# Performance work log

Measured on AMD Instinct MI355X. Metric: run time of the kernel, lower is better.

## Reference

```python
import jax, jax.numpy as jnp
import numpy as np

B, S, D, H, HD, FF, L, NF, NC, DH = 262144, 6, 16, 4, 4, 64, 10, 6, 139, 32
EPS = 1e-5

def _ln(x, w, b):
    m = x.mean(-1, keepdims=True)
    v = ((x - m) ** 2).mean(-1, keepdims=True)
    return (x - m) / jnp.sqrt(v + EPS) * w + b

def setup_inputs() -> dict:
    key = jax.random.key(0)
    ks = iter(jax.random.split(key, 64))
    def rn(shape, s=0.1):
        return jax.random.normal(next(ks), shape, jnp.float32) * s
    inp = {
        'feature_ids': jax.random.randint(next(ks), (B, S), 0, NF, jnp.int32),
        'feature_values': jax.random.normal(next(ks), (B, S, 1), jnp.float32),
        'mask': jnp.ones((B, S), bool),
        'type_embed': rn((NF, D), 1.0),
        'value_w': rn((D, 1)), 'value_b': rn((D,)),
        'pos_enc': rn((NF, D), 1.0),
        'qkv_w': rn((2, 3 * D, D)), 'qkv_b': rn((2, 3 * D)),
        'out_w': rn((2, D, D)), 'out_b': rn((2, D)),
        'ln1_w': jnp.ones((2, D)), 'ln1_b': jnp.zeros((2, D)),
        'ffn_w1': rn((2, FF, D)), 'ffn_b1': rn((2, FF)),
        'ffn_w2': rn((2, D, FF)), 'ffn_b2': rn((2, D)),
        'ln2_w': jnp.ones((2, D)), 'ln2_b': jnp.zeros((2, D)),
        'pool_w': rn((D, D)), 'pool_b': rn((D,)),
        'mu_w': rn((L, D)), 'mu_b': rn((L,)),
        'lv_w': rn((L, D)), 'lv_b': rn((L,)),
        'dec_w1': rn((NF, DH, L)), 'dec_b1': rn((NF, DH)),
        'dec_w2': rn((NF, 1, DH)), 'dec_b2': rn((NF, 1)),
        'cls_w1': rn((32, L)), 'cls_b1': rn((32,)),
        'cls_w2': rn((NC, 32)), 'cls_b2': rn((NC,)),
    }
    return inp

def _forward(feature_ids, feature_values, mask, type_embed, value_w, value_b, pos_enc,
             qkv_w, qkv_b, out_w, out_b, ln1_w, ln1_b, ffn_w1, ffn_b1, ffn_w2, ffn_b2,
             ln2_w, ln2_b, pool_w, pool_b, mu_w, mu_b, lv_w, lv_b,
             dec_w1, dec_b1, dec_w2, dec_b2, cls_w1, cls_b1, cls_w2, cls_b2):
    x = type_embed[feature_ids] + feature_values @ value_w.T + value_b  # (B,S,D)
    x = x + pos_enc[None, :S]
    maskf = mask.astype(x.dtype)
    bias = jnp.where(mask, 0.0, -1e9)[:, None, None, :]  # (B,1,1,S)
    for l in range(2):
        qkv = x @ qkv_w[l].T + qkv_b[l]
        q, k, v = jnp.split(qkv, 3, axis=-1)
        q = q.reshape(B, S, H, HD).transpose(0, 2, 1, 3)
        k = k.reshape(B, S, H, HD).transpose(0, 2, 1, 3)
        v = v.reshape(B, S, H, HD).transpose(0, 2, 1, 3)
        sc = jnp.einsum('bhqd,bhkd->bhqk', q, k) / jnp.sqrt(jnp.float32(HD))
        a = jax.nn.softmax(sc + bias, axis=-1)
        o = jnp.einsum('bhqk,bhkd->bhqd', a, v).transpose(0, 2, 1, 3).reshape(B, S, D)
        x = _ln(x + (o @ out_w[l].T + out_b[l]), ln1_w[l], ln1_b[l])
        f = jax.nn.relu(x @ ffn_w1[l].T + ffn_b1[l]) @ ffn_w2[l].T + ffn_b2[l]
        x = _ln(x + f, ln2_w[l], ln2_b[l])
    pooled = (x * maskf[..., None]).sum(1) / maskf.sum(1, keepdims=True)
    pooled = jax.nn.relu(pooled @ pool_w.T + pool_b)
    mu = pooled @ mu_w.T + mu_b
    logvar = pooled @ lv_w.T + lv_b
    eps = jax.random.normal(jax.random.key(42), mu.shape, mu.dtype)
    z = mu + eps * jnp.exp(0.5 * logvar)
    # run all 6 tiny decoders densely, then gather per feature_id (same math as per-token dispatch)
    h = jax.nn.relu(jnp.einsum('ehl,bl->beh', dec_w1, z) + dec_b1)      # (B,6,DH)
    allo = jnp.einsum('eoh,beh->beo', dec_w2, h)[..., 0] + dec_b2[:, 0]  # (B,6)
    recons = jnp.take_along_axis(allo, feature_ids, axis=1)[..., None]   # (B,S,1)
    logits = jax.nn.relu(z @ cls_w1.T + cls_b1) @ cls_w2.T + cls_b2
    return recons, mu, logvar, logits

def reference(feature_ids, feature_values, mask, type_embed, value_w, value_b, pos_enc,
              qkv_w, qkv_b, out_w, out_b, ln1_w, ln1_b, ffn_w1, ffn_b1, ffn_w2, ffn_b2,
              ln2_w, ln2_b, pool_w, pool_b, mu_w, mu_b, lv_w, lv_b,
              dec_w1, dec_b1, dec_w2, dec_b2, cls_w1, cls_b1, cls_w2, cls_b2):
    return _forward(feature_ids, feature_values, mask, type_embed, value_w, value_b, pos_enc,
                    qkv_w, qkv_b, out_w, out_b, ln1_w, ln1_b, ffn_w1, ffn_b1, ffn_w2, ffn_b2,
                    ln2_w, ln2_b, pool_w, pool_b, mu_w, mu_b, lv_w, lv_b,
                    dec_w1, dec_b1, dec_w2, dec_b2, cls_w1, cls_b1, cls_w2, cls_b2)
```

## Files before the change

kernel.cpp:

```cpp
#include <hip/hip_runtime.h>

#define DEVINL __device__ __forceinline__

constexpr int B  = 262144;
constexpr int S  = 6;
constexpr int NC = 139;

typedef _Float16 h2v __attribute__((ext_vector_type(2)));

constexpr int OUTB  = 0;
constexpr int LN1W  = 32;
constexpr int LN1B  = 64;
constexpr int LN2W  = 96;
constexpr int LN2B  = 128;
constexpr int QKVB  = 160;
constexpr int FF1B  = 256;
constexpr int FF2B  = 384;
constexpr int POOLB = 416;
constexpr int MUB   = 432;
constexpr int LVB   = 444;
constexpr int CL1B  = 456;
constexpr int CL2B  = 488;
constexpr int DEC1B = 628;
constexpr int DEC2W = 820;
constexpr int DEC2B = 1012;
constexpr int VALW  = 1020;
constexpr int VALB  = 1036;
constexpr int HQKV  = 1052;
constexpr int HOUT  = 1820;
constexpr int HFF1  = 2076;
constexpr int HFF2  = 3100;
constexpr int HPOOL = 4124;
constexpr int HMUW  = 4252;
constexpr int HLVW  = 4332;
constexpr int HCL1  = 4412;
constexpr int HCL2  = 4668;
constexpr int HDEC1 = 6892;
constexpr int WS_FLOATS = 8428;

#define LD4(off) (*reinterpret_cast<const float4*>(&smem[(off)]))
#define LD2(off) (*reinterpret_cast<const float2*>(&smem[(off)]))
#define BCH(f)   __builtin_bit_cast(h2v, (f))
#define BCF(h)   __builtin_bit_cast(float, (h))
#define FDOT2(a, b, c) __builtin_amdgcn_fdot2((a), (b), (c), false)

DEVINL h2v mkh2(float a, float b) { h2v r; r.x = (_Float16)a; r.y = (_Float16)b; return r; }
DEVINL h2v pkrtz(float a, float b) {
  return __builtin_bit_cast(h2v, __builtin_amdgcn_cvt_pkrtz(a, b));
}

#define DOTH_3(xh, bas, acc) do {                                    \
  const float4 wa_ = LD4(bas);                                       \
  const float4 wb_ = LD4((bas) + 4);                                 \
  const h2v w0_ = BCH(wa_.x), w1_ = BCH(wa_.y), w2_ = BCH(wa_.z), w3_ = BCH(wa_.w); \
  const h2v w4_ = BCH(wb_.x), w5_ = BCH(wb_.y), w6_ = BCH(wb_.z), w7_ = BCH(wb_.w); \
  _Pragma("unroll")                                                  \
  for (int r_ = 0; r_ < 3; ++r_) {                                   \
    acc[r_] = FDOT2(xh[r_][0], w0_, acc[r_]);                        \
    acc[r_] = FDOT2(xh[r_][1], w1_, acc[r_]);                        \
    acc[r_] = FDOT2(xh[r_][2], w2_, acc[r_]);                        \
    acc[r_] = FDOT2(xh[r_][3], w3_, acc[r_]);                        \
    acc[r_] = FDOT2(xh[r_][4], w4_, acc[r_]);                        \
    acc[r_] = FDOT2(xh[r_][5], w5_, acc[r_]);                        \
    acc[r_] = FDOT2(xh[r_][6], w6_, acc[r_]);                        \
    acc[r_] = FDOT2(xh[r_][7], w7_, acc[r_]);                        \
  }                                                                  \
} while (0)

#define DOT8H(vh, bas, acc) do {                                     \
  const float4 wa_ = LD4(bas);                                       \
  const float4 wb_ = LD4((bas) + 4);                                 \
  acc = FDOT2(vh[0], BCH(wa_.x), acc);                               \
  acc = FDOT2(vh[1], BCH(wa_.y), acc);                               \
  acc = FDOT2(vh[2], BCH(wa_.z), acc);                               \
  acc = FDOT2(vh[3], BCH(wa_.w), acc);                               \
  acc = FDOT2(vh[4], BCH(wb_.x), acc);                               \
  acc = FDOT2(vh[5], BCH(wb_.y), acc);                               \
  acc = FDOT2(vh[6], BCH(wb_.z), acc);                               \
  acc = FDOT2(vh[7], BCH(wb_.w), acc);                               \
} while (0)

DEVINL float dppswap(float v) {
  return __int_as_float(__builtin_amdgcn_mov_dpp(__float_as_int(v), 0xB1, 0xF, 0xF, true));
}

DEVINL float jax_normal_part(unsigned i) {
  const unsigned k1 = 42u;
  const unsigned k2 = 0x1BD11BDAu ^ 42u;
  unsigned x0 = 0u;
  unsigned x1 = i + k1;
#define TFR(r) { x0 += x1; x1 = (x1 << (r)) | (x1 >> (32 - (r))); x1 ^= x0; }
  TFR(13) TFR(15) TFR(26) TFR(6)
  x0 += k1; x1 += k2 + 1u;
  TFR(17) TFR(29) TFR(16) TFR(24)
  x0 += k2; x1 += 0u + 2u;
  TFR(13) TFR(15) TFR(26) TFR(6)
  x0 += 0u; x1 += k1 + 3u;
  TFR(17) TFR(29) TFR(16) TFR(24)
  x0 += k1; x1 += k2 + 4u;
  TFR(13) TFR(15) TFR(26) TFR(6)
  x0 += k2; x1 += 0u + 5u;
#undef TFR
  unsigned bits = x0 ^ x1;
  unsigned fb = (bits >> 9) | 0x3f800000u;
  float f = __uint_as_float(fb) - 1.0f;
  const float lo = -0.99999994f;
  float u = fmaxf(lo, fmaf(f, 2.0f, lo));
  float w = -log1pf(-u * u);
  float p;
  if (w < 5.0f) {
    w -= 2.5f;
    p =  2.81022636e-08f;
    p = fmaf(p, w,  3.43273939e-07f);
    p = fmaf(p, w, -3.5233877e-06f);
    p = fmaf(p, w, -4.39150654e-06f);
    p = fmaf(p, w,  0.00021858087f);
    p = fmaf(p, w, -0.00125372503f);
    p = fmaf(p, w, -0.00417768164f);
    p = fmaf(p, w,  0.246640727f);
    p = fmaf(p, w,  1.50140941f);
  } else {
    w = sqrtf(w) - 3.0f;
    p = -0.000200214257f;
    p = fmaf(p, w,  0.000100950558f);
    p = fmaf(p, w,  0.00134934322f);
    p = fmaf(p, w, -0.00367342844f);
    p = fmaf(p, w,  0.00573950773f);
    p = fmaf(p, w, -0.0076224613f);
    p = fmaf(p, w,  0.00943887047f);
    p = fmaf(p, w,  1.00167406f);
    p = fmaf(p, w,  2.83297682f);
  }
  return 1.41421356237f * (p * u);
}

__global__ __launch_bounds__(256, 2) void vae_fwd(
    const int*   __restrict__ feature_ids,
    const float* __restrict__ feature_values,
    const float* __restrict__ type_embed,
    const float* __restrict__ value_w,
    const float* __restrict__ value_b,
    const float* __restrict__ pos_enc,
    const float* __restrict__ qkv_w,
    const float* __restrict__ qkv_b,
    const float* __restrict__ out_w,
    const float* __restrict__ out_b,
    const float* __restrict__ ln1_w, const float* __restrict__ ln1_b,
    const float* __restrict__ ffn_w1,
    const float* __restrict__ ffn_b1,
    const float* __restrict__ ffn_w2,
    const float* __restrict__ ffn_b2,
    const float* __restrict__ ln2_w, const float* __restrict__ ln2_b,
    const float* __restrict__ pool_w,
    const float* __restrict__ pool_b,
    const float* __restrict__ mu_w, const float* __restrict__ mu_b,
    const float* __restrict__ lv_w, const float* __restrict__ lv_b,
    const float* __restrict__ dec_w1,
    const float* __restrict__ dec_b1,
    const float* __restrict__ dec_w2,
    const float* __restrict__ dec_b2,
    const float* __restrict__ cls_w1,
    const float* __restrict__ cls_b1,
    const float* __restrict__ cls_w2,
    const float* __restrict__ cls_b2,
    float*       __restrict__ out)
{
  __shared__ __align__(16) float smem[WS_FLOATS];

  {
    const int t = threadIdx.x;
#define CP(dst, src, n) for (int i_ = t; i_ < (n); i_ += 256) smem[(dst) + i_] = (src)[i_]
#define CPH(dst, src, n) for (int i_ = t; i_ < (n); i_ += 256) \
    smem[(dst) + i_] = BCF(mkh2((src)[2 * i_], (src)[2 * i_ + 1]))
    CP(OUTB, out_b, 32);
    CP(LN1W, ln1_w, 32);  CP(LN1B, ln1_b, 32);
    CP(LN2W, ln2_w, 32);  CP(LN2B, ln2_b, 32);
    CP(QKVB, qkv_b, 96);
    CP(FF1B, ffn_b1, 128); CP(FF2B, ffn_b2, 32);
    CP(POOLB, pool_b, 16);
    CP(MUB, mu_b, 10);    CP(LVB, lv_b, 10);
    CP(CL1B, cls_b1, 32); CP(CL2B, cls_b2, 139);
    CP(DEC1B, dec_b1, 192); CP(DEC2W, dec_w2, 192); CP(DEC2B, dec_b2, 6);
    CP(VALW, value_w, 16); CP(VALB, value_b, 16);
    CPH(HQKV, qkv_w, 768);
    CPH(HOUT, out_w, 256);
    CPH(HFF1, ffn_w1, 1024);
    CPH(HFF2, ffn_w2, 1024);
    CPH(HPOOL, pool_w, 128);
    CPH(HMUW, mu_w, 80);
    CPH(HLVW, lv_w, 80);
    CPH(HCL2, cls_w2, 2224);
    for (int idx = t; idx < 256; idx += 256) {
      int row = idx >> 3, k = idx & 7;
      float a = (k < 5) ? cls_w1[row * 10 + 2 * k] : 0.f;
      float b = (k < 5) ? cls_w1[row * 10 + 2 * k + 1] : 0.f;
      smem[HCL1 + idx] = BCF(mkh2(a, b));
    }
    for (int idx = t; idx < 1536; idx += 256) {
      int row = idx >> 3, k = idx & 7;
      float a = (k < 5) ? dec_w1[row * 10 + 2 * k] : 0.f;
      float b = (k < 5) ? dec_w1[row * 10 + 2 * k + 1] : 0.f;
      smem[HDEC1 + idx] = BCF(mkh2(a, b));
    }
#undef CP
#undef CPH
  }
  __syncthreads();

  const int tid  = blockIdx.x * 256 + threadIdx.x;
  const int elem = tid >> 1;
  const int sub  = tid & 1;
  const bool his = (sub != 0);

  float x[3][16];
  int   fid[3];
#pragma unroll
  for (int i = 0; i < 3; ++i) {
    const int r = sub * 3 + i;
    fid[i] = feature_ids[elem * S + r];
    const float fv = feature_values[elem * S + r];
    const float* te = type_embed + fid[i] * 16;
    const float* pe = pos_enc + r * 16;
#pragma unroll
    for (int d = 0; d < 16; ++d)
      x[i][d] = te[d] + fv * smem[VALW + d] + smem[VALB + d] + pe[d];
  }

#pragma unroll 1
  for (int l = 0; l < 2; ++l) {
    const int WqH = HQKV + l * 384;
    const int bqO = QKVB + l * 48;
    const int WoH = HOUT + l * 128;
    const int w1H = HFF1 + l * 512;
    const int b1O = FF1B + l * 64;
    const int w2H = HFF2 + l * 512;
    const int b2O = FF2B + l * 16;

    h2v xh[3][8];
#pragma unroll
    for (int r = 0; r < 3; ++r)
#pragma unroll
      for (int k = 0; k < 8; ++k) xh[r][k] = pkrtz(x[r][2 * k], x[r][2 * k + 1]);

    float y[3][16];
#pragma unroll
    for (int r = 0; r < 3; ++r)
#pragma unroll
      for (int j = 0; j < 16; ++j) y[r][j] = x[r][j] + smem[OUTB + l * 16 + j];

#pragma unroll 1
    for (int h = 0; h < 4; ++h) {
      float qq[4][3], kk[4][3];
#pragma unroll
      for (int e = 0; e < 4; ++e) {
        float bq0 = smem[bqO + h * 4 + e];
        float bk0 = smem[bqO + 16 + h * 4 + e];
        float aq[3] = {bq0, bq0, bq0};
        float ak[3] = {bk0, bk0, bk0};
        DOTH_3(xh, WqH + (h * 4 + e) * 8, aq);
        DOTH_3(xh, WqH + (16 + h * 4 + e) * 8, ak);
#pragma unroll
        for (int r = 0; r < 3; ++r) { qq[e][r] = aq[r] * 0.5f; kk[e][r] = ak[r]; }
      }

      h2v qp[3][2], kpo[3][2], kpp[3][2];
#pragma unroll
      for (int r = 0; r < 3; ++r) {
        qp[r][0] = pkrtz(qq[0][r], qq[1][r]);
        qp[r][1] = pkrtz(qq[2][r], qq[3][r]);
      }
#pragma unroll
      for (int i = 0; i < 3; ++i) {
        kpo[i][0] = pkrtz(kk[0][i], kk[1][i]);
        kpo[i][1] = pkrtz(kk[2][i], kk[3][i]);
        kpp[i][0] = BCH(dppswap(BCF(kpo[i][0])));
        kpp[i][1] = BCH(dppswap(BCF(kpo[i][1])));
      }

      float scO[3][3], scP[3][3];
#pragma unroll
      for (int r = 0; r < 3; ++r)
#pragma unroll
        for (int i = 0; i < 3; ++i) {
          scO[r][i] = FDOT2(qp[r][1], kpo[i][1], FDOT2(qp[r][0], kpo[i][0], 0.f));
          scP[r][i] = FDOT2(qp[r][1], kpp[i][1], FDOT2(qp[r][0], kpp[i][0], 0.f));
        }

#pragma unroll
      for (int r = 0; r < 3; ++r) {
        float mx = scO[r][0];
#pragma unroll
        for (int i = 1; i < 3; ++i) mx = fmaxf(mx, scO[r][i]);
#pragma unroll
        for (int i = 0; i < 3; ++i) mx = fmaxf(mx, scP[r][i]);
        float den = 0.f;
#pragma unroll
        for (int i = 0; i < 3; ++i) { scO[r][i] = __expf(scO[r][i] - mx); den += scO[r][i]; }
#pragma unroll
        for (int i = 0; i < 3; ++i) { scP[r][i] = __expf(scP[r][i] - mx); den += scP[r][i]; }
        const float inv = 1.0f / den;
#pragma unroll
        for (int i = 0; i < 3; ++i) { scO[r][i] *= inv; scP[r][i] *= inv; }
      }

      float vv[4][3];
#pragma unroll
      for (int e = 0; e < 4; ++e) {
        float bv0 = smem[bqO + 32 + h * 4 + e];
        float av[3] = {bv0, bv0, bv0};
        DOTH_3(xh, WqH + (32 + h * 4 + e) * 8, av);
#pragma unroll
        for (int r = 0; r < 3; ++r) vv[e][r] = av[r];
      }

      h2v vp0[4], vp1[4], vp2[4];
#pragma unroll
      for (int e = 0; e < 4; ++e) {
        const float q0 = dppswap(vv[e][0]);
        const float q1 = dppswap(vv[e][1]);
        const float q2 = dppswap(vv[e][2]);
        vp0[e] = pkrtz(vv[e][0], vv[e][1]);
        vp1[e] = pkrtz(vv[e][2], q0);
        vp2[e] = pkrtz(q1, q2);
      }
      h2v sp0[3], sp1[3], sp2[3];
#pragma unroll
      for (int r = 0; r < 3; ++r) {
        sp0[r] = pkrtz(scO[r][0], scO[r][1]);
        sp1[r] = pkrtz(scO[r][2], scP[r][0]);
        sp2[r] = pkrtz(scP[r][1], scP[r][2]);
      }
      float oh[3][4];
#pragma unroll
      for (int r = 0; r < 3; ++r)
#pragma unroll
        for (int e = 0; e < 4; ++e)
          oh[r][e] = FDOT2(sp2[r], vp2[e], FDOT2(sp1[r], vp1[e], FDOT2(sp0[r], vp0[e], 0.f)));

      h2v ohp[3][2];
#pragma unroll
      for (int r = 0; r < 3; ++r) {
        ohp[r][0] = pkrtz(oh[r][0], oh[r][1]);
        ohp[r][1] = pkrtz(oh[r][2], oh[r][3]);
      }
      const int wbase = WoH + h * 2;
#pragma unroll
      for (int j = 0; j < 16; ++j) {
        const float2 w = LD2(wbase + j * 8);
        const h2v w0 = BCH(w.x), w1 = BCH(w.y);
#pragma unroll
        for (int r = 0; r < 3; ++r)
          y[r][j] = FDOT2(ohp[r][1], w1, FDOT2(ohp[r][0], w0, y[r][j]));
      }
    }

#pragma unroll
    for (int r = 0; r < 3; ++r) {
      float m = 0.f;
#pragma unroll
      for (int d = 0; d < 16; ++d) m += y[r][d];
      m *= 0.0625f;
      float var = 0.f;
#pragma unroll
      for (int d = 0; d < 16; ++d) { float dd = y[r][d] - m; var = fmaf(dd, dd, var); }
      var *= 0.0625f;
      float rr = 1.0f / sqrtf(var + 1e-5f);
#pragma unroll
      for (int d = 0; d < 16; ++d)
        y[r][d] = (y[r][d] - m) * rr * smem[LN1W + l * 16 + d] + smem[LN1B + l * 16 + d];
    }

    h2v yh[3][8];
#pragma unroll
    for (int r = 0; r < 3; ++r)
#pragma unroll
      for (int k = 0; k < 8; ++k) yh[r][k] = pkrtz(y[r][2 * k], y[r][2 * k + 1]);

    float t2[3][16];
#pragma unroll
    for (int r = 0; r < 3; ++r)
#pragma unroll
      for (int j = 0; j < 16; ++j) t2[r][j] = y[r][j] + smem[b2O + j];

#pragma unroll 1
    for (int fo = 0; fo < 4; ++fo) {
      h2v hch[3][8];
#pragma unroll
      for (int m2 = 0; m2 < 8; ++m2) {
        float b0 = smem[b1O + fo * 16 + 2 * m2];
        float b1v = smem[b1O + fo * 16 + 2 * m2 + 1];
        float a0[3] = {b0, b0, b0};
        float a1[3] = {b1v, b1v, b1v};
        DOTH_3(yh, w1H + (fo * 16 + 2 * m2) * 8, a0);
        DOTH_3(yh, w1H + (fo * 16 + 2 * m2 + 1) * 8, a1);
#pragma unroll
        for (int r = 0; r < 3; ++r)
          hch[r][m2] = pkrtz(fmaxf(a0[r], 0.f), fmaxf(a1[r], 0.f));
      }
#pragma unroll
      for (int j = 0; j < 16; ++j) {
        const int bas = w2H + j * 32 + fo * 8;
        float a[3] = {t2[0][j], t2[1][j], t2[2][j]};
        DOTH_3(hch, bas, a);
        t2[0][j] = a[0]; t2[1][j] = a[1]; t2[2][j] = a[2];
      }
    }
#pragma unroll
    for (int r = 0; r < 3; ++r) {
      float m = 0.f;
#pragma unroll
      for (int d = 0; d < 16; ++d) m += t2[r][d];
      m *= 0.0625f;
      float var = 0.f;
#pragma unroll
      for (int d = 0; d < 16; ++d) { float dd = t2[r][d] - m; var = fmaf(dd, dd, var); }
      var *= 0.0625f;
      float rr = 1.0f / sqrtf(var + 1e-5f);
#pragma unroll
      for (int d = 0; d < 16; ++d)
        x[r][d] = (t2[r][d] - m) * rr * smem[LN2W + l * 16 + d] + smem[LN2B + l * 16 + d];
    }
  }

  float pooled[16];
#pragma unroll
  for (int d = 0; d < 16; ++d) {
    float v = x[0][d] + x[1][d] + x[2][d];
    v += dppswap(v);
    pooled[d] = v * (1.0f / 6.0f);
  }
  h2v ph[8];
#pragma unroll
  for (int k = 0; k < 8; ++k) ph[k] = pkrtz(pooled[2 * k], pooled[2 * k + 1]);

  float pp[16];
#pragma unroll
  for (int jj = 0; jj < 8; ++jj) {
    const int j = sub * 8 + jj;
    float a = smem[POOLB + j];
    DOT8H(ph, HPOOL + j * 8, a);
    a = fmaxf(a, 0.f);
    const float o = dppswap(a);
    pp[jj]     = his ? o : a;
    pp[8 + jj] = his ? a : o;
  }
  h2v pph[8];
#pragma unroll
  for (int k = 0; k < 8; ++k) pph[k] = pkrtz(pp[2 * k], pp[2 * k + 1]);

  float* muo = out + (size_t)B * 6;
  float* lvo = out + (size_t)B * 16;
  float z5[5];
#pragma unroll
  for (int jj = 0; jj < 5; ++jj) {
    const int j = sub * 5 + jj;
    float mu = smem[MUB + j], lv = smem[LVB + j];
    DOT8H(pph, HMUW + j * 8, mu);
    DOT8H(pph, HLVW + j * 8, lv);
    const float eps = jax_normal_part((unsigned)elem * 10u + (unsigned)j);
    z5[jj] = fmaf(eps, __expf(0.5f * lv), mu);
    muo[(size_t)elem * 10 + j] = mu;
    lvo[(size_t)elem * 10 + j] = lv;
  }

  float z[10];
#pragma unroll
  for (int jj = 0; jj < 5; ++jj) {
    const float o = dppswap(z5[jj]);
    z[jj]     = his ? o : z5[jj];
    z[5 + jj] = his ? z5[jj] : o;
  }
  h2v zh8[8];
#pragma unroll
  for (int k = 0; k < 5; ++k) zh8[k] = pkrtz(z[2 * k], z[2 * k + 1]);
  zh8[5] = pkrtz(0.f, 0.f); zh8[6] = zh8[5]; zh8[7] = zh8[5];

  float h2[32];
#pragma unroll
  for (int ii = 0; ii < 16; ++ii) {
    const int i = sub * 16 + ii;
    float a = smem[CL1B + i];
    DOT8H(zh8, HCL1 + i * 8, a);
    a = fmaxf(a, 0.f);
    const float o = dppswap(a);
    h2[ii]      = his ? o : a;
    h2[16 + ii] = his ? a : o;
  }
  h2v hh[16];
#pragma unroll
  for (int k = 0; k < 16; ++k) hh[k] = pkrtz(h2[2 * k], h2[2 * k + 1]);

  float* lgo = out + (size_t)B * 26;
#pragma unroll 2
  for (int cc = 0; cc < 70; ++cc) {
    const int c = cc * 2 + sub;
    if (c < NC) {
      const int bas = HCL2 + c * 16;
      float a = smem[CL2B + c];
#pragma unroll
      for (int q4 = 0; q4 < 4; ++q4) {
        const float4 w = LD4(bas + q4 * 4);
        a = FDOT2(hh[q4 * 4 + 0], BCH(w.x), a);
        a = FDOT2(hh[q4 * 4 + 1], BCH(w.y), a);
        a = FDOT2(hh[q4 * 4 + 2], BCH(w.z), a);
        a = FDOT2(hh[q4 * 4 + 3], BCH(w.w), a);
      }
      lgo[(size_t)elem * 139 + c] = a;
    }
  }

  float accd[3];
#pragma unroll
  for (int i = 0; i < 3; ++i) {
    const int e = sub * 3 + i;
    float acc = smem[DEC2B + e];
#pragma unroll 2
    for (int dd = 0; dd < 32; ++dd) {
      float a = smem[DEC1B + e * 32 + dd];
      DOT8H(zh8, HDEC1 + (e * 32 + dd) * 8, a);
      acc = fmaf(fmaxf(a, 0.f), smem[DEC2W + e * 32 + dd], acc);
    }
    accd[i] = acc;
  }
  float alo[3], ahi[3];
#pragma unroll
  for (int i = 0; i < 3; ++i) {
    const float o = dppswap(accd[i]);
    alo[i] = his ? o : accd[i];
    ahi[i] = his ? accd[i] : o;
  }
#pragma unroll
  for (int i = 0; i < 3; ++i) {
    const int f = fid[i];
    float v = alo[0];
    v = (f == 1) ? alo[1] : v;
    v = (f == 2) ? alo[2] : v;
    v = (f == 3) ? ahi[0] : v;
    v = (f == 4) ? ahi[1] : v;
    v = (f == 5) ? ahi[2] : v;
    out[(size_t)elem * 6 + sub * 3 + i] = v;
  }
}

extern "C" void kernel_launch(void* const* d_in, const int* in_sizes, int n_in,
                              void* d_out, int out_size, void* d_ws, size_t ws_size,
                              hipStream_t stream) {
  (void)in_sizes; (void)n_in; (void)d_ws; (void)ws_size; (void)out_size;
  const int*   feature_ids    = (const int*)  d_in[0];
  const float* feature_values = (const float*)d_in[1];
  const float* type_embed = (const float*)d_in[3];
  const float* value_w    = (const float*)d_in[4];
  const float* value_b    = (const float*)d_in[5];
  const float* pos_enc    = (const float*)d_in[6];
  const float* qkv_w      = (const float*)d_in[7];
  const float* qkv_b      = (const float*)d_in[8];
  const float* out_w      = (const float*)d_in[9];
  const float* out_b      = (const float*)d_in[10];
  const float* ln1_w      = (const float*)d_in[11];
  const float* ln1_b      = (const float*)d_in[12];
  const float* ffn_w1     = (const float*)d_in[13];
  const float* ffn_b1     = (const float*)d_in[14];
  const float* ffn_w2     = (const float*)d_in[15];
  const float* ffn_b2     = (const float*)d_in[16];
  const float* ln2_w      = (const float*)d_in[17];
  const float* ln2_b      = (const float*)d_in[18];
  const float* pool_w     = (const float*)d_in[19];
  const float* pool_b     = (const float*)d_in[20];
  const float* mu_w       = (const float*)d_in[21];
  const float* mu_b       = (const float*)d_in[22];
  const float* lv_w       = (const float*)d_in[23];
  const float* lv_b       = (const float*)d_in[24];
  const float* dec_w1     = (const float*)d_in[25];
  const float* dec_b1     = (const float*)d_in[26];
  const float* dec_w2     = (const float*)d_in[27];
  const float* dec_b2     = (const float*)d_in[28];
  const float* cls_w1     = (const float*)d_in[29];
  const float* cls_b1     = (const float*)d_in[30];
  const float* cls_w2     = (const float*)d_in[31];
  const float* cls_b2     = (const float*)d_in[32];
  float* outp = (float*)d_out;

  const int threads = 256;
  const int blocks  = (B * 2) / threads;
  vae_fwd<<<blocks, threads, 0, stream>>>(
      feature_ids, feature_values, type_embed, value_w, value_b, pos_enc,
      qkv_w, qkv_b, out_w, out_b, ln1_w, ln1_b, ffn_w1, ffn_b1, ffn_w2, ffn_b2,
      ln2_w, ln2_b, pool_w, pool_b, mu_w, mu_b, lv_w, lv_b,
      dec_w1, dec_b1, dec_w2, dec_b2, cls_w1, cls_b1, cls_w2, cls_b2, outp);
}
```

Before: 294.2 us.

## Prepack classifier and decoder fp16 weights into global workspace, read via cache

Adds a small prepack kernel that converts cls_w2 and dec_w1 to packed fp16 in the workspace buffer. The main kernel now reads these weights from global memory (L1/L2 cached) instead of staging them in LDS. This roughly halves shared memory per block, which cuts per-block staging work and may raise occupancy. The cost is that the hot classifier and decoder loops now issue global vector loads instead of LDS reads, and there is an extra kernel launch.

After: 307.0 us. 1.04x slower.

```diff
diff --git a/kernel.cpp b/kernel.cpp
--- a/kernel.cpp
+++ b/kernel.cpp
@@ -34,9 +34,11 @@
 constexpr int HMUW  = 4252;
 constexpr int HLVW  = 4332;
 constexpr int HCL1  = 4412;
-constexpr int HCL2  = 4668;
-constexpr int HDEC1 = 6892;
-constexpr int WS_FLOATS = 8428;
+constexpr int WS_FLOATS = 4668;
+
+constexpr int WSCL2  = 0;
+constexpr int WSDEC1 = 2224;
+constexpr int WS_U32 = 3760;
 
 #define LD4(off) (*reinterpret_cast<const float4*>(&smem[(off)]))
 #define LD2(off) (*reinterpret_cast<const float2*>(&smem[(off)]))
@@ -70,6 +72,19 @@
 #define DOT8H(vh, bas, acc) do {                                     \
   const float4 wa_ = LD4(bas);                                       \
   const float4 wb_ = LD4((bas) + 4);                                 \
+  acc = FDOT2(vh[0], BCH(wa_.x), acc);                               \
+  acc = FDOT2(vh[1], BCH(wa_.y), acc);                               \
+  acc = FDOT2(vh[2], BCH(wa_.z), acc);                               \
+  acc = FDOT2(vh[3], BCH(wa_.w), acc);                               \
+  acc = FDOT2(vh[4], BCH(wb_.x), acc);                               \
+  acc = FDOT2(vh[5], BCH(wb_.y), acc);                               \
+  acc = FDOT2(vh[6], BCH(wb_.z), acc);                               \
+  acc = FDOT2(vh[7], BCH(wb_.w), acc);                               \
+} while (0)
+
+#define DOT8G(vh, p, acc) do {                                       \
+  const float4 wa_ = (p)[0];                                         \
+  const float4 wb_ = (p)[1];                                         \
   acc = FDOT2(vh[0], BCH(wa_.x), acc);                               \
   acc = FDOT2(vh[1], BCH(wa_.y), acc);                               \
   acc = FDOT2(vh[2], BCH(wa_.z), acc);                               \
@@ -134,6 +149,22 @@
   return 1.41421356237f * (p * u);
 }
 
+__global__ __launch_bounds__(256) void prepack_ws(
+    const float* __restrict__ cls_w2,
+    const float* __restrict__ dec_w1,
+    unsigned*    __restrict__ ws)
+{
+  const int t = blockIdx.x * 256 + threadIdx.x;
+  for (int i = t; i < 2224; i += 2048)
+    ws[WSCL2 + i] = __builtin_bit_cast(unsigned, mkh2(cls_w2[2 * i], cls_w2[2 * i + 1]));
+  for (int i = t; i < 1536; i += 2048) {
+    int row = i >> 3, k = i & 7;
+    float a = (k < 5) ? dec_w1[row * 10 + 2 * k] : 0.f;
+    float b = (k < 5) ? dec_w1[row * 10 + 2 * k + 1] : 0.f;
+    ws[WSDEC1 + i] = __builtin_bit_cast(unsigned, mkh2(a, b));
+  }
+}
+
 __global__ __launch_bounds__(256, 2) void vae_fwd(
     const int*   __restrict__ feature_ids,
     const float* __restrict__ feature_values,
@@ -155,14 +186,13 @@
     const float* __restrict__ pool_b,
     const float* __restrict__ mu_w, const float* __restrict__ mu_b,
     const float* __restrict__ lv_w, const float* __restrict__ lv_b,
-    const float* __restrict__ dec_w1,
     const float* __restrict__ dec_b1,
     const float* __restrict__ dec_w2,
     const float* __restrict__ dec_b2,
     const float* __restrict__ cls_w1,
     const float* __restrict__ cls_b1,
-    const float* __restrict__ cls_w2,
     const float* __restrict__ cls_b2,
+    const unsigned* __restrict__ wsp,
     float*       __restrict__ out)
 {
   __shared__ __align__(16) float smem[WS_FLOATS];
@@ -189,18 +219,11 @@
     CPH(HPOOL, pool_w, 128);
     CPH(HMUW, mu_w, 80);
     CPH(HLVW, lv_w, 80);
-    CPH(HCL2, cls_w2, 2224);
     for (int idx = t; idx < 256; idx += 256) {
       int row = idx >> 3, k = idx & 7;
       float a = (k < 5) ? cls_w1[row * 10 + 2 * k] : 0.f;
       float b = (k < 5) ? cls_w1[row * 10 + 2 * k + 1] : 0.f;
       smem[HCL1 + idx] = BCF(mkh2(a, b));
-    }
-    for (int idx = t; idx < 1536; idx += 256) {
-      int row = idx >> 3, k = idx & 7;
-      float a = (k < 5) ? dec_w1[row * 10 + 2 * k] : 0.f;
-      float b = (k < 5) ? dec_w1[row * 10 + 2 * k + 1] : 0.f;
-      smem[HDEC1 + idx] = BCF(mkh2(a, b));
     }
 #undef CP
 #undef CPH
@@ -495,11 +518,11 @@
   for (int cc = 0; cc < 70; ++cc) {
     const int c = cc * 2 + sub;
     if (c < NC) {
-      const int bas = HCL2 + c * 16;
+      const float4* wr = reinterpret_cast<const float4*>(wsp + WSCL2 + c * 16);
       float a = smem[CL2B + c];
 #pragma unroll
       for (int q4 = 0; q4 < 4; ++q4) {
-        const float4 w = LD4(bas + q4 * 4);
+        const float4 w = wr[q4];
         a = FDOT2(hh[q4 * 4 + 0], BCH(w.x), a);
         a = FDOT2(hh[q4 * 4 + 1], BCH(w.y), a);
         a = FDOT2(hh[q4 * 4 + 2], BCH(w.z), a);
@@ -516,8 +539,9 @@
     float acc = smem[DEC2B + e];
 #pragma unroll 2
     for (int dd = 0; dd < 32; ++dd) {
+      const float4* dr = reinterpret_cast<const float4*>(wsp + WSDEC1 + (e * 32 + dd) * 8);
       float a = smem[DEC1B + e * 32 + dd];
-      DOT8H(zh8, HDEC1 + (e * 32 + dd) * 8, a);
+      DOT8G(zh8, dr, a);
       acc = fmaf(fmaxf(a, 0.f), smem[DEC2W + e * 32 + dd], acc);
     }
     accd[i] = acc;
@@ -545,7 +569,7 @@
 extern "C" void kernel_launch(void* const* d_in, const int* in_sizes, int n_in,
                               void* d_out, int out_size, void* d_ws, size_t ws_size,
                               hipStream_t stream) {
-  (void)in_sizes; (void)n_in; (void)d_ws; (void)ws_size; (void)out_size;
+  (void)in_sizes; (void)n_in; (void)ws_size; (void)out_size;
   const int*   feature_ids    = (const int*)  d_in[0];
   const float* feature_values = (const float*)d_in[1];
   const float* type_embed = (const float*)d_in[3];
@@ -579,6 +603,9 @@
   const float* cls_w2     = (const float*)d_in[31];
   const float* cls_b2     = (const float*)d_in[32];
   float* outp = (float*)d_out;
+  unsigned* wsp = (unsigned*)d_ws;
+
+  prepack_ws<<<8, 256, 0, stream>>>(cls_w2, dec_w1, wsp);
 
   const int threads = 256;
   const int blocks  = (B * 2) / threads;
@@ -586,5 +613,5 @@
       feature_ids, feature_values, type_embed, value_w, value_b, pos_enc,
       qkv_w, qkv_b, out_w, out_b, ln1_w, ln1_b, ffn_w1, ffn_b1, ffn_w2, ffn_b2,
       ln2_w, ln2_b, pool_w, pool_b, mu_w, mu_b, lv_w, lv_b,
-      dec_w1, dec_b1, dec_w2, dec_b2, cls_w1, cls_b1, cls_w2, cls_b2, outp);
+      dec_b1, dec_w2, dec_b2, cls_w1, cls_b1, cls_b2, wsp, outp);
 }
```
